# Kernel tuning notes

Measured on AMD Instinct MI355X. Metric: run time of the kernel, lower is better.

## Reference

```python
import jax, jax.numpy as jnp
import numpy as np

B, S, H, NH = 2, 2048, 2048, 16
HD = H // NH


def setup_inputs() -> dict:
    key = jax.random.key(0)
    ks = jax.random.split(key, 9)
    s = 1.0 / np.sqrt(H)
    return {
        "hidden_state": jax.random.normal(ks[0], (B, S, H), dtype=jnp.float32),
        "Wq": jax.random.normal(ks[1], (H, H), dtype=jnp.float32) * s,
        "bq": jnp.zeros((H,), dtype=jnp.float32),
        "Wk": jax.random.normal(ks[2], (H, H), dtype=jnp.float32) * s,
        "bk": jnp.zeros((H,), dtype=jnp.float32),
        "Wv": jax.random.normal(ks[3], (H, H), dtype=jnp.float32) * s,
        "bv": jnp.zeros((H,), dtype=jnp.float32),
        "Wo": jax.random.normal(ks[4], (H, H), dtype=jnp.float32) * s,
        "bo": jnp.zeros((H,), dtype=jnp.float32),
    }


def _split_heads(x):
    # [B,S,H] -> [B,NH,S,HD]
    b, s, _ = x.shape
    return x.reshape(b, s, NH, HD).transpose(0, 2, 1, 3)


def reference(hidden_state, Wq, bq, Wk, bk, Wv, bv, Wo, bo):
    q = _split_heads(hidden_state @ Wq.T + bq)
    k = _split_heads(hidden_state @ Wk.T + bk)
    v = _split_heads(hidden_state @ Wv.T + bv)
    scale = 1.0 / jnp.sqrt(jnp.array(HD, dtype=q.dtype))
    scores = jnp.einsum("bhqd,bhkd->bhqk", q, k) * scale
    attn = jax.nn.softmax(scores, axis=-1)
    out = jnp.einsum("bhqk,bhkd->bhqd", attn, v)  # [B,NH,S,HD]
    out = out.transpose(0, 2, 1, 3).reshape(hidden_state.shape[0], -1, H)
    return out @ Wo.T + bo
```

## Files before the change

kernel.cpp:

```cpp
#include <hip/hip_runtime.h>
#include <hip/hip_bf16.h>
#include <stdint.h>

#define B_ 2
#define S_ 2048
#define H_ 2048
#define NH_ 16
#define HD_ 128
#define M_ (B_*S_)

typedef __attribute__((ext_vector_type(8))) short short8_t;
typedef __attribute__((ext_vector_type(4))) float floatx4;
typedef __attribute__((ext_vector_type(16))) float floatx16;

__device__ __forceinline__ short f2bf(float f) {
  union { float f; uint32_t u; } x; x.f = f;
  const uint32_t u = x.u;
  return (short)((u + 0x7FFFu + ((u >> 16) & 1u)) >> 16);
}

__device__ __forceinline__ void gload_lds16(const void* g, void* l) {
  __builtin_amdgcn_global_load_lds(
      (const __attribute__((address_space(1))) void*)g,
      (__attribute__((address_space(3))) void*)l, 16, 0, 0);
}

__global__ __launch_bounds__(256)
void cast_all(const float* __restrict__ h,  const float* __restrict__ wq,
              const float* __restrict__ wk, const float* __restrict__ wv,
              const float* __restrict__ wo,
              short* __restrict__ hB,  short* __restrict__ wqB,
              short* __restrict__ wkB, short* __restrict__ wvB,
              short* __restrict__ woB) {
  const int blk = blockIdx.x;
  const float* src; short* dst; int off;
  if      (blk <  4096) { src = h;  dst = hB;  off = blk; }
  else if (blk <  6144) { src = wq; dst = wqB; off = blk - 4096; }
  else if (blk <  8192) { src = wk; dst = wkB; off = blk - 6144; }
  else if (blk < 10240) { src = wv; dst = wvB; off = blk - 8192; }
  else                  { src = wo; dst = woB; off = blk - 10240; }
  const int i = (off * 256 + threadIdx.x) * 8;
  typedef __attribute__((ext_vector_type(4))) float f4;
  const f4 a = *(const f4*)(src + i);
  const f4 b = *(const f4*)(src + i + 4);
  short8_t o;
  o[0] = f2bf(a[0]); o[1] = f2bf(a[1]); o[2] = f2bf(a[2]); o[3] = f2bf(a[3]);
  o[4] = f2bf(b[0]); o[5] = f2bf(b[1]); o[6] = f2bf(b[2]); o[7] = f2bf(b[3]);
  *(short8_t*)(dst + i) = o;
}

template<int MODE>
__device__ __forceinline__
void gemm_body(const short* __restrict__ A, const short* __restrict__ Bm,
               const float* __restrict__ bias, void* __restrict__ C,
               const int m0, const int n0, const int N, const int K) {
  __shared__ short As[128 * 64];
  __shared__ short Bs[128 * 64];
  const int tid = threadIdx.x;
  const int wv = tid >> 6, ln = tid & 63;
  const int lr = ln >> 4, lc = ln & 15;
  const int wm = (wv >> 1) * 64, wn = (wv & 1) * 64;
  const int srow = ln >> 3;
  const int sc   = (ln & 7) ^ srow;

  floatx4 acc[4][4] = {};
  const short* aP[4];
  const short* bP[4];
#pragma unroll
  for (int i = 0; i < 4; ++i)
    aP[i] = A + (size_t)(m0 + wv * 32 + i * 8 + srow) * K + sc * 8;
#pragma unroll
  for (int i = 0; i < 4; ++i)
    bP[i] = Bm + (size_t)(n0 + wv * 32 + i * 8 + srow) * K + sc * 8;
  const int sw = (lc & 7) << 3;

  for (int k0 = 0; k0 < K; k0 += 64) {
#pragma unroll
    for (int i = 0; i < 4; ++i)
      gload_lds16(aP[i] + k0, &As[(wv * 32 + i * 8) * 64]);
#pragma unroll
    for (int i = 0; i < 4; ++i)
      gload_lds16(bP[i] + k0, &Bs[(wv * 32 + i * 8) * 64]);
    __syncthreads();
#pragma unroll
    for (int ksq = 0; ksq < 2; ++ksq) {
      short8_t af[4], bf[4];
#pragma unroll
      for (int t = 0; t < 4; ++t)
        af[t] = *(const short8_t*)&As[(wm + t * 16 + lc) * 64 + ((ksq * 32 + lr * 8) ^ sw)];
#pragma unroll
      for (int t = 0; t < 4; ++t)
        bf[t] = *(const short8_t*)&Bs[(wn + t * 16 + lc) * 64 + ((ksq * 32 + lr * 8) ^ sw)];
#pragma unroll
      for (int i = 0; i < 4; ++i)
#pragma unroll
        for (int j = 0; j < 4; ++j)
          acc[i][j] = __builtin_amdgcn_mfma_f32_16x16x32_bf16(af[i], bf[j], acc[i][j], 0, 0, 0);
    }
    __syncthreads();
  }

#pragma unroll
  for (int i = 0; i < 4; ++i) {
#pragma unroll
    for (int j = 0; j < 4; ++j) {
      const int col = n0 + wn + j * 16 + lc;
      const float bv = bias[col];
#pragma unroll
      for (int r = 0; r < 4; ++r) {
        const int row = m0 + wm + i * 16 + lr * 4 + r;
        const float v = acc[i][j][r] + bv;
        if (MODE == 1) ((float*)C)[(size_t)row * N + col] = v;
        else           ((short*)C)[(size_t)row * N + col] = f2bf(v);
      }
    }
  }
}

__global__ __launch_bounds__(256)
void gemm_qkv(const short* __restrict__ A,
              const short* __restrict__ W0, const short* __restrict__ W1, const short* __restrict__ W2,
              const float* __restrict__ b0, const float* __restrict__ b1, const float* __restrict__ b2,
              short* __restrict__ C0, short* __restrict__ C1, short* __restrict__ C2) {
  const int sel = blockIdx.x >> 4;
  const short* Bm   = sel == 0 ? W0 : (sel == 1 ? W1 : W2);
  const float* bias = sel == 0 ? b0 : (sel == 1 ? b1 : b2);
  short* C          = sel == 0 ? C0 : (sel == 1 ? C1 : C2);
  gemm_body<0>(A, Bm, bias, C, blockIdx.y * 128, (blockIdx.x & 15) * 128, H_, H_);
}

__global__ __launch_bounds__(256)
void gemm_out(const short* __restrict__ A, const short* __restrict__ Bm,
              const float* __restrict__ bias, float* __restrict__ C) {
  gemm_body<1>(A, Bm, bias, C, blockIdx.y * 128, blockIdx.x * 128, H_, H_);
}

__global__ __launch_bounds__(256)
void arrange_v(const short* __restrict__ V, short* __restrict__ Vt) {
  __shared__ short T[64][72];
  const int b = blockIdx.z;
  const int s0 = blockIdx.x * 64, c0 = blockIdx.y * 64;
  const int t = threadIdx.x;
  const int r = t >> 3, c8 = (t & 7) * 8;
  const int kt = s0 >> 6;
#pragma unroll
  for (int p = 0; p < 2; ++p) {
    const int row = p * 32 + r;
    *(short8_t*)&T[row][c8] =
        *(const short8_t*)&V[(size_t)(b * S_ + s0 + row) * H_ + c0 + c8];
  }
  __syncthreads();
#pragma unroll
  for (int p = 0; p < 2; ++p) {
    const int row = p * 32 + r;
    const int gcol = c0 + row;
    const int hh = gcol >> 7, d = gcol & 127;
    short8_t o;
#pragma unroll
    for (int j = 0; j < 8; ++j) o[j] = T[c8 + j][row];
    const int chunk = (c8 >> 3) ^ (d & 7);
    *(short8_t*)&Vt[((((size_t)(b * 16 + hh) * 32 + kt) * 128 + d) << 6) + chunk * 8] = o;
  }
}

__global__ __launch_bounds__(256, 2)
void attention(const short* __restrict__ Q, const short* __restrict__ Kg,
               const short* __restrict__ Vt, short* __restrict__ O) {
  __shared__ short Ks[64 * 128];
  __shared__ short Vs[128 * 64];
  __shared__ short Ps[128 * 64];

  const int tid = threadIdx.x;
  const int wv = tid >> 6, ln = tid & 63;
  const int l32 = ln & 31, lh = ln >> 5;
  const int bh = blockIdx.y, b = bh >> 4, h = bh & 15;
  const int qw = blockIdx.x * 128 + wv * 32;

  const short* Qp  = Q  + ((size_t)(b * S_ + qw)) * H_ + h * HD_;
  const short* VtB = Vt + (size_t)bh * (S_ * HD_) + (size_t)wv * 2048 + ln * 8;

  const short* kp[4];
#pragma unroll
  for (int j = 0; j < 4; ++j) {
    const int key = wv * 16 + j * 4 + (ln >> 4);
    const int sc = (ln & 15) ^ (key & 7);
    kp[j] = Kg + (size_t)(b * S_ + key) * H_ + h * HD_ + sc * 8;
  }

  short8_t qf[8];
#pragma unroll
  for (int ksq = 0; ksq < 8; ++ksq)
    qf[ksq] = *(const short8_t*)&Qp[(size_t)l32 * H_ + ksq * 16 + lh * 8];

  floatx16 oacc[4] = {};
  float lsum[16] = {};
  const float csc = 0.08838834764831845f * 1.4426950408889634f;

  for (int kt = 0; kt < S_ / 64; ++kt) {
    const size_t kadv = (size_t)kt * 64 * H_;
#pragma unroll
    for (int j = 0; j < 4; ++j)
      gload_lds16(kp[j] + kadv, &Ks[(wv * 16 + j * 4) * 128]);
#pragma unroll
    for (int j = 0; j < 4; ++j)
      gload_lds16(VtB + (size_t)kt * 8192 + j * 512, &Vs[wv * 2048 + j * 512]);
    __syncthreads();

    floatx16 sacc[2] = {};
#pragma unroll
    for (int kh = 0; kh < 2; ++kh) {
      const int key = kh * 32 + l32;
      const int swk = (key & 7) * 8;
#pragma unroll
      for (int ksq = 0; ksq < 8; ++ksq) {
        const short8_t kf =
            *(const short8_t*)&Ks[key * 128 + (((ksq * 2 + lh) * 8) ^ swk)];
        sacc[kh] = __builtin_amdgcn_mfma_f32_32x32x16_bf16(qf[ksq], kf, sacc[kh], 0, 0, 0);
      }
    }

#pragma unroll
    for (int kh = 0; kh < 2; ++kh) {
#pragma unroll
      for (int r = 0; r < 16; ++r) {
        const float p = exp2f(sacc[kh][r] * csc);
        const uint32_t u = __float_as_uint(p);
        const int row = wv * 32 + (r & 3) + 8 * (r >> 2) + 4 * lh;
        const int col = kh * 32 + l32;
        Ps[row * 64 + ((((col >> 3) ^ (row & 7)) * 8) | (col & 7))] = (short)(u >> 16);
        lsum[r] += __uint_as_float(u & 0xffff0000u);
      }
    }

    const int prow = wv * 32 + l32;
    const int swp = (prow & 7) * 8;
#pragma unroll
    for (int kf = 0; kf < 4; ++kf) {
      const short8_t pf =
          *(const short8_t*)&Ps[prow * 64 + (((kf * 2 + lh) * 8) ^ swp)];
#pragma unroll
      for (int dt = 0; dt < 4; ++dt) {
        const int d = dt * 32 + l32;
        const short8_t vf =
            *(const short8_t*)&Vs[d * 64 + (((kf * 2 + lh) * 8) ^ ((d & 7) * 8))];
        oacc[dt] = __builtin_amdgcn_mfma_f32_32x32x16_bf16(pf, vf, oacc[dt], 0, 0, 0);
      }
    }
    __syncthreads();
  }

  float inv[16];
#pragma unroll
  for (int r = 0; r < 16; ++r) {
    float l = lsum[r];
    l += __shfl_xor(l, 1);
    l += __shfl_xor(l, 2);
    l += __shfl_xor(l, 4);
    l += __shfl_xor(l, 8);
    l += __shfl_xor(l, 16);
    inv[r] = 1.0f / l;
  }
  short* Op = O + ((size_t)(b * S_ + qw)) * H_ + h * HD_;
#pragma unroll
  for (int dt = 0; dt < 4; ++dt)
#pragma unroll
    for (int r = 0; r < 16; ++r) {
      const int rowl = (r & 3) + 8 * (r >> 2) + 4 * lh;
      Op[(size_t)rowl * H_ + dt * 32 + l32] = f2bf(oacc[dt][r] * inv[r]);
    }
}

extern "C" void kernel_launch(void* const* d_in, const int* in_sizes, int n_in,
                              void* d_out, int out_size, void* d_ws, size_t ws_size,
                              hipStream_t stream) {
  const float* hidden = (const float*)d_in[0];
  const float* Wq = (const float*)d_in[1];
  const float* bq = (const float*)d_in[2];
  const float* Wk = (const float*)d_in[3];
  const float* bk = (const float*)d_in[4];
  const float* Wv = (const float*)d_in[5];
  const float* bv = (const float*)d_in[6];
  const float* Wo = (const float*)d_in[7];
  const float* bo = (const float*)d_in[8];
  float* out = (float*)d_out;

  char* ws = (char*)d_ws;
  short* hB  = (short*)(ws);
  short* WqB = (short*)(ws + (16u << 20));
  short* WkB = (short*)(ws + (24u << 20));
  short* WvB = (short*)(ws + (32u << 20));
  short* WoB = (short*)(ws + (40u << 20));
  short* Qb  = (short*)(ws + (48u << 20));
  short* Kb  = (short*)(ws + (64u << 20));
  short* Vb  = (short*)(ws + (80u << 20));
  short* Vtb = (short*)(ws + (96u << 20));
  short* Ob  = (short*)(ws + (112u << 20));

  cast_all<<<12288, 256, 0, stream>>>(hidden, Wq, Wk, Wv, Wo, hB, WqB, WkB, WvB, WoB);

  gemm_qkv<<<dim3(48, M_ / 128), 256, 0, stream>>>(hB, WqB, WkB, WvB, bq, bk, bv, Qb, Kb, Vb);

  arrange_v<<<dim3(S_ / 64, H_ / 64, B_), 256, 0, stream>>>(Vb, Vtb);

  attention<<<dim3(S_ / 128, B_ * NH_), 256, 0, stream>>>(Qb, Kb, Vtb, Ob);

  gemm_out<<<dim3(H_ / 128, M_ / 128), 256, 0, stream>>>(Ob, WoB, bo, out);
}
```

Baseline: 395.4 us.

## Load K and V fragments directly from global memory instead of LDS staging

The attention kernel no longer stages K and V tiles into shared memory with global_load_lds. Each wave now reads its MFMA K and V fragments straight from global memory into registers, and the block-wide barriers are dropped, since each wave reads only its own rows of Ps. To give V a plain per-head transposed layout [bh][d][S], arrange_v is rewritten to drop the swizzled tile layout. This removes LDS traffic and barrier stalls, but the four waves now fetch the same K/V redundantly through the caches, with strided global accesses and memory latency exposed in the inner loop.

Measured after the change: 535.8 us. +35.5%, slower.

```diff
diff --git a/kernel.cpp b/kernel.cpp
--- a/kernel.cpp
+++ b/kernel.cpp
@@ -142,7 +142,6 @@
   const int s0 = blockIdx.x * 64, c0 = blockIdx.y * 64;
   const int t = threadIdx.x;
   const int r = t >> 3, c8 = (t & 7) * 8;
-  const int kt = s0 >> 6;
 #pragma unroll
   for (int p = 0; p < 2; ++p) {
     const int row = p * 32 + r;
@@ -158,16 +157,13 @@
     short8_t o;
 #pragma unroll
     for (int j = 0; j < 8; ++j) o[j] = T[c8 + j][row];
-    const int chunk = (c8 >> 3) ^ (d & 7);
-    *(short8_t*)&Vt[((((size_t)(b * 16 + hh) * 32 + kt) * 128 + d) << 6) + chunk * 8] = o;
+    *(short8_t*)&Vt[((size_t)(b * 16 + hh) * 128 + d) * S_ + s0 + c8] = o;
   }
 }
 
 __global__ __launch_bounds__(256, 2)
 void attention(const short* __restrict__ Q, const short* __restrict__ Kg,
                const short* __restrict__ Vt, short* __restrict__ O) {
-  __shared__ short Ks[64 * 128];
-  __shared__ short Vs[128 * 64];
   __shared__ short Ps[128 * 64];
 
   const int tid = threadIdx.x;
@@ -176,16 +172,9 @@
   const int bh = blockIdx.y, b = bh >> 4, h = bh & 15;
   const int qw = blockIdx.x * 128 + wv * 32;
 
-  const short* Qp  = Q  + ((size_t)(b * S_ + qw)) * H_ + h * HD_;
-  const short* VtB = Vt + (size_t)bh * (S_ * HD_) + (size_t)wv * 2048 + ln * 8;
-
-  const short* kp[4];
-#pragma unroll
-  for (int j = 0; j < 4; ++j) {
-    const int key = wv * 16 + j * 4 + (ln >> 4);
-    const int sc = (ln & 15) ^ (key & 7);
-    kp[j] = Kg + (size_t)(b * S_ + key) * H_ + h * HD_ + sc * 8;
-  }
+  const short* Qp = Q  + ((size_t)(b * S_ + qw)) * H_ + h * HD_;
+  const short* Kp = Kg + (size_t)(b * S_ + l32) * H_ + h * HD_ + lh * 8;
+  const short* Vp = Vt + ((size_t)bh * HD_ + l32) * S_ + lh * 8;
 
   short8_t qf[8];
 #pragma unroll
@@ -196,25 +185,19 @@
   float lsum[16] = {};
   const float csc = 0.08838834764831845f * 1.4426950408889634f;
 
+  const int prow = wv * 32 + l32;
+  const int swp = (prow & 7) * 8;
+
   for (int kt = 0; kt < S_ / 64; ++kt) {
-    const size_t kadv = (size_t)kt * 64 * H_;
-#pragma unroll
-    for (int j = 0; j < 4; ++j)
-      gload_lds16(kp[j] + kadv, &Ks[(wv * 16 + j * 4) * 128]);
-#pragma unroll
-    for (int j = 0; j < 4; ++j)
-      gload_lds16(VtB + (size_t)kt * 8192 + j * 512, &Vs[wv * 2048 + j * 512]);
-    __syncthreads();
+    const int key0 = kt * 64;
 
     floatx16 sacc[2] = {};
 #pragma unroll
     for (int kh = 0; kh < 2; ++kh) {
-      const int key = kh * 32 + l32;
-      const int swk = (key & 7) * 8;
+      const short* kRow = Kp + (size_t)(key0 + kh * 32) * H_;
 #pragma unroll
       for (int ksq = 0; ksq < 8; ++ksq) {
-        const short8_t kf =
-            *(const short8_t*)&Ks[key * 128 + (((ksq * 2 + lh) * 8) ^ swk)];
+        const short8_t kf = *(const short8_t*)&kRow[ksq * 16];
         sacc[kh] = __builtin_amdgcn_mfma_f32_32x32x16_bf16(qf[ksq], kf, sacc[kh], 0, 0, 0);
       }
     }
@@ -232,21 +215,17 @@
       }
     }
 
-    const int prow = wv * 32 + l32;
-    const int swp = (prow & 7) * 8;
 #pragma unroll
     for (int kf = 0; kf < 4; ++kf) {
       const short8_t pf =
           *(const short8_t*)&Ps[prow * 64 + (((kf * 2 + lh) * 8) ^ swp)];
 #pragma unroll
       for (int dt = 0; dt < 4; ++dt) {
-        const int d = dt * 32 + l32;
         const short8_t vf =
-            *(const short8_t*)&Vs[d * 64 + (((kf * 2 + lh) * 8) ^ ((d & 7) * 8))];
+            *(const short8_t*)&Vp[(size_t)dt * 32 * S_ + key0 + kf * 16];
         oacc[dt] = __builtin_amdgcn_mfma_f32_32x32x16_bf16(pf, vf, oacc[dt], 0, 0, 0);
       }
     }
-    __syncthreads();
   }
 
   float inv[16];
```

## Double-buffer attention K/V tiles and split-K the output projection

Applied to the files above, without the earlier changes.

The attention kernel now keeps two LDS buffers for the K and V tiles. It prefetches the next tile right after a single per-iteration barrier, so global-to-LDS loads overlap the MFMA work, and one of the two barriers per iteration is removed. The output GEMM is split into two K-halves that write fp32 partials into reused workspace. A new reduce kernel then adds the two partials and the bias. This doubles the block count for the output GEMM, at the cost of extra partial-buffer memory traffic and an additional kernel launch. Attention LDS use rises to 80KB per block.

New measurement: 435.8 us. 1.1x slower.

```diff
diff --git a/kernel.cpp b/kernel.cpp
--- a/kernel.cpp
+++ b/kernel.cpp
@@ -53,7 +53,7 @@
 __device__ __forceinline__
 void gemm_body(const short* __restrict__ A, const short* __restrict__ Bm,
                const float* __restrict__ bias, void* __restrict__ C,
-               const int m0, const int n0, const int N, const int K) {
+               const int m0, const int n0, const int N, const int K, const int ldk) {
   __shared__ short As[128 * 64];
   __shared__ short Bs[128 * 64];
   const int tid = threadIdx.x;
@@ -68,10 +68,10 @@
   const short* bP[4];
 #pragma unroll
   for (int i = 0; i < 4; ++i)
-    aP[i] = A + (size_t)(m0 + wv * 32 + i * 8 + srow) * K + sc * 8;
+    aP[i] = A + (size_t)(m0 + wv * 32 + i * 8 + srow) * ldk + sc * 8;
 #pragma unroll
   for (int i = 0; i < 4; ++i)
-    bP[i] = Bm + (size_t)(n0 + wv * 32 + i * 8 + srow) * K + sc * 8;
+    bP[i] = Bm + (size_t)(n0 + wv * 32 + i * 8 + srow) * ldk + sc * 8;
   const int sw = (lc & 7) << 3;
 
   for (int k0 = 0; k0 < K; k0 += 64) {
@@ -105,13 +105,13 @@
 #pragma unroll
     for (int j = 0; j < 4; ++j) {
       const int col = n0 + wn + j * 16 + lc;
-      const float bv = bias[col];
+      const float bv = (MODE == 2) ? 0.f : bias[col];
 #pragma unroll
       for (int r = 0; r < 4; ++r) {
         const int row = m0 + wm + i * 16 + lr * 4 + r;
         const float v = acc[i][j][r] + bv;
-        if (MODE == 1) ((float*)C)[(size_t)row * N + col] = v;
-        else           ((short*)C)[(size_t)row * N + col] = f2bf(v);
+        if (MODE == 0) ((short*)C)[(size_t)row * N + col] = f2bf(v);
+        else           ((float*)C)[(size_t)row * N + col] = v;
       }
     }
   }
@@ -126,13 +126,29 @@
   const short* Bm   = sel == 0 ? W0 : (sel == 1 ? W1 : W2);
   const float* bias = sel == 0 ? b0 : (sel == 1 ? b1 : b2);
   short* C          = sel == 0 ? C0 : (sel == 1 ? C1 : C2);
-  gemm_body<0>(A, Bm, bias, C, blockIdx.y * 128, (blockIdx.x & 15) * 128, H_, H_);
-}
-
-__global__ __launch_bounds__(256)
-void gemm_out(const short* __restrict__ A, const short* __restrict__ Bm,
-              const float* __restrict__ bias, float* __restrict__ C) {
-  gemm_body<1>(A, Bm, bias, C, blockIdx.y * 128, blockIdx.x * 128, H_, H_);
+  gemm_body<0>(A, Bm, bias, C, blockIdx.y * 128, (blockIdx.x & 15) * 128, H_, H_, H_);
+}
+
+__global__ __launch_bounds__(256)
+void gemm_out_splitk(const short* __restrict__ A, const short* __restrict__ Bm,
+                     float* __restrict__ P0, float* __restrict__ P1) {
+  const int z = blockIdx.z;
+  float* P = z ? P1 : P0;
+  gemm_body<2>(A + z * 1024, Bm + z * 1024, nullptr, P,
+               blockIdx.y * 128, blockIdx.x * 128, H_, 1024, H_);
+}
+
+__global__ __launch_bounds__(256)
+void reduce_out(const float* __restrict__ P0, const float* __restrict__ P1,
+                const float* __restrict__ bias, float* __restrict__ out) {
+  typedef __attribute__((ext_vector_type(4))) float f4;
+  const int i = (blockIdx.x * 256 + threadIdx.x) * 8;
+  const int col = i & (H_ - 1);
+  const f4 a0 = *(const f4*)(P0 + i),   a1 = *(const f4*)(P0 + i + 4);
+  const f4 b0 = *(const f4*)(P1 + i),   b1 = *(const f4*)(P1 + i + 4);
+  const f4 c0 = *(const f4*)(bias + col), c1 = *(const f4*)(bias + col + 4);
+  *(f4*)(out + i)     = a0 + b0 + c0;
+  *(f4*)(out + i + 4) = a1 + b1 + c1;
 }
 
 __global__ __launch_bounds__(256)
@@ -166,8 +182,8 @@
 __global__ __launch_bounds__(256, 2)
 void attention(const short* __restrict__ Q, const short* __restrict__ Kg,
                const short* __restrict__ Vt, short* __restrict__ O) {
-  __shared__ short Ks[64 * 128];
-  __shared__ short Vs[128 * 64];
+  __shared__ short Ks[2][64 * 128];
+  __shared__ short Vs[2][128 * 64];
   __shared__ short Ps[128 * 64];
 
   const int tid = threadIdx.x;
@@ -196,15 +212,26 @@
   float lsum[16] = {};
   const float csc = 0.08838834764831845f * 1.4426950408889634f;
 
+#pragma unroll
+  for (int j = 0; j < 4; ++j)
+    gload_lds16(kp[j], &Ks[0][(wv * 16 + j * 4) * 128]);
+#pragma unroll
+  for (int j = 0; j < 4; ++j)
+    gload_lds16(VtB + j * 512, &Vs[0][wv * 2048 + j * 512]);
+
   for (int kt = 0; kt < S_ / 64; ++kt) {
-    const size_t kadv = (size_t)kt * 64 * H_;
-#pragma unroll
-    for (int j = 0; j < 4; ++j)
-      gload_lds16(kp[j] + kadv, &Ks[(wv * 16 + j * 4) * 128]);
-#pragma unroll
-    for (int j = 0; j < 4; ++j)
-      gload_lds16(VtB + (size_t)kt * 8192 + j * 512, &Vs[wv * 2048 + j * 512]);
+    const int cur = kt & 1;
     __syncthreads();
+
+    if (kt + 1 < S_ / 64) {
+      const size_t kadv = (size_t)(kt + 1) * 64 * H_;
+#pragma unroll
+      for (int j = 0; j < 4; ++j)
+        gload_lds16(kp[j] + kadv, &Ks[cur ^ 1][(wv * 16 + j * 4) * 128]);
+#pragma unroll
+      for (int j = 0; j < 4; ++j)
+        gload_lds16(VtB + (size_t)(kt + 1) * 8192 + j * 512, &Vs[cur ^ 1][wv * 2048 + j * 512]);
+    }
 
     floatx16 sacc[2] = {};
 #pragma unroll
@@ -214,7 +241,7 @@
 #pragma unroll
       for (int ksq = 0; ksq < 8; ++ksq) {
         const short8_t kf =
-            *(const short8_t*)&Ks[key * 128 + (((ksq * 2 + lh) * 8) ^ swk)];
+            *(const short8_t*)&Ks[cur][key * 128 + (((ksq * 2 + lh) * 8) ^ swk)];
         sacc[kh] = __builtin_amdgcn_mfma_f32_32x32x16_bf16(qf[ksq], kf, sacc[kh], 0, 0, 0);
       }
     }
@@ -242,11 +269,10 @@
       for (int dt = 0; dt < 4; ++dt) {
         const int d = dt * 32 + l32;
         const short8_t vf =
-            *(const short8_t*)&Vs[d * 64 + (((kf * 2 + lh) * 8) ^ ((d & 7) * 8))];
+            *(const short8_t*)&Vs[cur][d * 64 + (((kf * 2 + lh) * 8) ^ ((d & 7) * 8))];
         oacc[dt] = __builtin_amdgcn_mfma_f32_32x32x16_bf16(pf, vf, oacc[dt], 0, 0, 0);
       }
     }
-    __syncthreads();
   }
 
   float inv[16];
@@ -295,6 +321,8 @@
   short* Vb  = (short*)(ws + (80u << 20));
   short* Vtb = (short*)(ws + (96u << 20));
   short* Ob  = (short*)(ws + (112u << 20));
+  float* P0  = (float*)(ws + (48u << 20));
+  float* P1  = (float*)(ws + (80u << 20));
 
   cast_all<<<12288, 256, 0, stream>>>(hidden, Wq, Wk, Wv, Wo, hB, WqB, WkB, WvB, WoB);
 
@@ -304,5 +332,7 @@
 
   attention<<<dim3(S_ / 128, B_ * NH_), 256, 0, stream>>>(Qb, Kb, Vtb, Ob);
 
-  gemm_out<<<dim3(H_ / 128, M_ / 128), 256, 0, stream>>>(Ob, WoB, bo, out);
-}
+  gemm_out_splitk<<<dim3(H_ / 128, M_ / 128, 2), 256, 0, stream>>>(Ob, WoB, P0, P1);
+
+  reduce_out<<<M_ * H_ / 2048, 256, 0, stream>>>(P0, P1, bo, out);
+}
```

## Double-buffer K/V tiles and keep P in registers via transposed QK MFMA

Applied to the files above, without the earlier changes.

Adds ping-pong LDS buffers for K and V so the next tile's global-to-LDS loads are issued before the current tile's compute, and drops the trailing barrier. It also swaps the MFMA operands so that S^T lands with keys in the accumulator layout. P is then packed into bf16 pairs and rearranged across half-waves with shuffles to form the PV A-operand, which removes the Ps LDS round-trip. The row sum becomes a single per-lane scalar that is reduced at the end through a small LDS array. The cost is that the double buffer doubles K/V LDS use, and the single barrier per iteration must still protect buffer reuse. The final invLds read happens without a barrier, but each wave writes and reads only its own rows, so it is likely fine.

Measured after the change: 391.3 us. Within noise of the previous version (-1.0%).

```diff
diff --git a/kernel.cpp b/kernel.cpp
--- a/kernel.cpp
+++ b/kernel.cpp
@@ -166,9 +166,9 @@
 __global__ __launch_bounds__(256, 2)
 void attention(const short* __restrict__ Q, const short* __restrict__ Kg,
                const short* __restrict__ Vt, short* __restrict__ O) {
-  __shared__ short Ks[64 * 128];
-  __shared__ short Vs[128 * 64];
-  __shared__ short Ps[128 * 64];
+  __shared__ short Ks[2][64 * 128];
+  __shared__ short Vs[2][128 * 64];
+  __shared__ float invLds[128];
 
   const int tid = threadIdx.x;
   const int wv = tid >> 6, ln = tid & 63;
@@ -193,18 +193,29 @@
     qf[ksq] = *(const short8_t*)&Qp[(size_t)l32 * H_ + ksq * 16 + lh * 8];
 
   floatx16 oacc[4] = {};
-  float lsum[16] = {};
+  float lsum = 0.f;
   const float csc = 0.08838834764831845f * 1.4426950408889634f;
 
+#pragma unroll
+  for (int j = 0; j < 4; ++j)
+    gload_lds16(kp[j], &Ks[0][(wv * 16 + j * 4) * 128]);
+#pragma unroll
+  for (int j = 0; j < 4; ++j)
+    gload_lds16(VtB + j * 512, &Vs[0][wv * 2048 + j * 512]);
+
   for (int kt = 0; kt < S_ / 64; ++kt) {
-    const size_t kadv = (size_t)kt * 64 * H_;
-#pragma unroll
-    for (int j = 0; j < 4; ++j)
-      gload_lds16(kp[j] + kadv, &Ks[(wv * 16 + j * 4) * 128]);
-#pragma unroll
-    for (int j = 0; j < 4; ++j)
-      gload_lds16(VtB + (size_t)kt * 8192 + j * 512, &Vs[wv * 2048 + j * 512]);
+    const int cur = kt & 1;
     __syncthreads();
+
+    if (kt + 1 < S_ / 64) {
+      const size_t kadv = (size_t)(kt + 1) * 64 * H_;
+#pragma unroll
+      for (int j = 0; j < 4; ++j)
+        gload_lds16(kp[j] + kadv, &Ks[cur ^ 1][(wv * 16 + j * 4) * 128]);
+#pragma unroll
+      for (int j = 0; j < 4; ++j)
+        gload_lds16(VtB + (size_t)(kt + 1) * 8192 + j * 512, &Vs[cur ^ 1][wv * 2048 + j * 512]);
+    }
 
     floatx16 sacc[2] = {};
 #pragma unroll
@@ -214,52 +225,54 @@
 #pragma unroll
       for (int ksq = 0; ksq < 8; ++ksq) {
         const short8_t kf =
-            *(const short8_t*)&Ks[key * 128 + (((ksq * 2 + lh) * 8) ^ swk)];
-        sacc[kh] = __builtin_amdgcn_mfma_f32_32x32x16_bf16(qf[ksq], kf, sacc[kh], 0, 0, 0);
+            *(const short8_t*)&Ks[cur][key * 128 + (((ksq * 2 + lh) * 8) ^ swk)];
+        sacc[kh] = __builtin_amdgcn_mfma_f32_32x32x16_bf16(kf, qf[ksq], sacc[kh], 0, 0, 0);
       }
     }
 
+    int pfr[4][4];
 #pragma unroll
     for (int kh = 0; kh < 2; ++kh) {
-#pragma unroll
-      for (int r = 0; r < 16; ++r) {
-        const float p = exp2f(sacc[kh][r] * csc);
-        const uint32_t u = __float_as_uint(p);
-        const int row = wv * 32 + (r & 3) + 8 * (r >> 2) + 4 * lh;
-        const int col = kh * 32 + l32;
-        Ps[row * 64 + ((((col >> 3) ^ (row & 7)) * 8) | (col & 7))] = (short)(u >> 16);
-        lsum[r] += __uint_as_float(u & 0xffff0000u);
+      uint32_t P[8];
+#pragma unroll
+      for (int i = 0; i < 8; ++i) {
+        const uint32_t u0 = __float_as_uint(exp2f(sacc[kh][2 * i] * csc));
+        const uint32_t u1 = __float_as_uint(exp2f(sacc[kh][2 * i + 1] * csc));
+        lsum += __uint_as_float(u0 & 0xffff0000u) + __uint_as_float(u1 & 0xffff0000u);
+        P[i] = (u0 >> 16) | (u1 & 0xffff0000u);
       }
-    }
-
-    const int prow = wv * 32 + l32;
-    const int swp = (prow & 7) * 8;
+#pragma unroll
+      for (int t = 0; t < 2; ++t)
+#pragma unroll
+        for (int j = 0; j < 2; ++j) {
+          const int a = (int)P[t * 4 + j], bb = (int)P[t * 4 + j + 2];
+          const int as = __shfl_xor(a, 32), bs = __shfl_xor(bb, 32);
+          pfr[kh * 2 + t][j]     = lh ? bs : a;
+          pfr[kh * 2 + t][j + 2] = lh ? bb : as;
+        }
+    }
+
 #pragma unroll
     for (int kf = 0; kf < 4; ++kf) {
-      const short8_t pf =
-          *(const short8_t*)&Ps[prow * 64 + (((kf * 2 + lh) * 8) ^ swp)];
+      union { int i[4]; short8_t s; } pu;
+#pragma unroll
+      for (int j = 0; j < 4; ++j) pu.i[j] = pfr[kf][j];
 #pragma unroll
       for (int dt = 0; dt < 4; ++dt) {
         const int d = dt * 32 + l32;
         const short8_t vf =
-            *(const short8_t*)&Vs[d * 64 + (((kf * 2 + lh) * 8) ^ ((d & 7) * 8))];
-        oacc[dt] = __builtin_amdgcn_mfma_f32_32x32x16_bf16(pf, vf, oacc[dt], 0, 0, 0);
+            *(const short8_t*)&Vs[cur][d * 64 + (((kf * 2 + lh) * 8) ^ ((d & 7) * 8))];
+        oacc[dt] = __builtin_amdgcn_mfma_f32_32x32x16_bf16(pu.s, vf, oacc[dt], 0, 0, 0);
       }
     }
-    __syncthreads();
-  }
-
+  }
+
+  const float l = lsum + __shfl_xor(lsum, 32);
+  invLds[wv * 32 + l32] = 1.0f / l;
   float inv[16];
 #pragma unroll
-  for (int r = 0; r < 16; ++r) {
-    float l = lsum[r];
-    l += __shfl_xor(l, 1);
-    l += __shfl_xor(l, 2);
-    l += __shfl_xor(l, 4);
-    l += __shfl_xor(l, 8);
-    l += __shfl_xor(l, 16);
-    inv[r] = 1.0f / l;
-  }
+  for (int r = 0; r < 16; ++r)
+    inv[r] = invLds[wv * 32 + (r & 3) + 8 * (r >> 2) + 4 * lh];
   short* Op = O + ((size_t)(b * S_ + qw)) * H_ + h * HD_;
 #pragma unroll
   for (int dt = 0; dt < 4; ++dt)
```
